# Optimization experiments

Hardware: AMD Instinct MI355X
Metric: run time of the kernel (lower is better)

Reference implementation:

```python
import jax, jax.numpy as jnp
import numpy as np

N = 20000      # nodes
E = 500000     # edges (~25 neighbors/node)
G = 64         # graphs in batch
NF = 64        # num_features (node dim)
NG = 100       # num_gaussians (edge dim)
L = 6          # conv layers
FC = 128       # fc_feat_size
NFC = 3        # num_fc_layers - 1
EMB = 92       # KHOT embedding width
CUTOFF = 6.0
EPS = 1e-5


def setup_inputs() -> dict:
    key = jax.random.key(0)
    ks = jax.random.split(key, 16)
    s = 0.05
    inp = {}
    inp['atomic_numbers'] = jax.random.randint(ks[0], (N,), 0, 100, dtype=jnp.int32)
    inp['neighbors_index'] = jax.random.randint(ks[1], (2, E), 0, N, dtype=jnp.int32)
    inp['distances'] = jax.random.uniform(ks[2], (E,), dtype=jnp.float32) * CUTOFF
    inp['batch'] = jnp.sort(jax.random.randint(ks[3], (N,), 0, G, dtype=jnp.int32))
    # parameters
    inp['embedding'] = jax.random.normal(ks[4], (100, EMB), jnp.float32) * s
    inp['nuc_W'] = jax.random.normal(ks[5], (EMB, NF), jnp.float32) * s
    inp['nuc_b'] = jnp.zeros((NF,), jnp.float32)
    inp['conv_W'] = jax.random.normal(ks[6], (L, 2 * NF + NG, 2 * NF), jnp.float32) * s
    inp['conv_b'] = jnp.zeros((L, 2 * NF), jnp.float32)
    inp['bn_g'] = jnp.ones((L, 2 * NF), jnp.float32)
    inp['bn_b'] = jnp.zeros((L, 2 * NF), jnp.float32)
    inp['ln_g'] = jnp.ones((L, NF), jnp.float32)
    inp['ln_b'] = jnp.zeros((L, NF), jnp.float32)
    inp['fc1_W'] = jax.random.normal(ks[7], (NF, FC), jnp.float32) * s
    inp['fc1_b'] = jnp.zeros((FC,), jnp.float32)
    inp['fcs_W'] = jax.random.normal(ks[8], (NFC, FC, FC), jnp.float32) * s
    inp['fcs_b'] = jnp.zeros((NFC, FC), jnp.float32)
    inp['out_W'] = jax.random.normal(ks[9], (FC, 1), jnp.float32) * s
    inp['out_b'] = jnp.zeros((1,), jnp.float32)
    return inp


def reference(atomic_numbers, neighbors_index, distances, batch,
              embedding, nuc_W, nuc_b, conv_W, conv_b, bn_g, bn_b,
              ln_g, ln_b, fc1_W, fc1_b, fcs_W, fcs_b, out_W, out_b):
    # Gaussian smearing of edge distances -> [E, NG]
    offsets = jnp.linspace(0.0, CUTOFF, NG)
    coeff = -0.5 / (offsets[1] - offsets[0]) ** 2
    ef = jnp.exp(coeff * (distances[:, None] - offsets) ** 2)

    # atom k-hot embedding -> nuclear linear embedding: [N, NF]
    x = embedding[atomic_numbers] @ nuc_W + nuc_b

    src, dst = neighbors_index[0], neighbors_index[1]  # x_j = src, x_i = dst

    for l in range(L):
        # edge message: gather + concat + linear
        z = jnp.concatenate([x[dst], x[src], ef], axis=1) @ conv_W[l] + conv_b[l]
        # BatchNorm1d over edges (training-mode batch statistics, biased var)
        mu = z.mean(axis=0)
        var = jnp.mean((z - mu) ** 2, axis=0)
        z = (z - mu) / jnp.sqrt(var + EPS) * bn_g[l] + bn_b[l]
        z1, z2 = jnp.split(z, 2, axis=1)
        m = jax.nn.sigmoid(z1) * jax.nn.softplus(z2)  # [E, NF]
        # scatter-add aggregate to target nodes
        agg = jax.ops.segment_sum(m, dst, num_segments=N)
        # LayerNorm + residual + softplus
        mu2 = agg.mean(axis=-1, keepdims=True)
        var2 = jnp.mean((agg - mu2) ** 2, axis=-1, keepdims=True)
        h = (agg - mu2) / jnp.sqrt(var2 + EPS) * ln_g[l] + ln_b[l]
        x = jax.nn.softplus(h + x)

    # mean pool per graph
    counts = jnp.maximum(jax.ops.segment_sum(jnp.ones((N,), x.dtype), batch, num_segments=G), 1.0)
    mol = jax.ops.segment_sum(x, batch, num_segments=G) / counts[:, None]

    h = jax.nn.softplus(mol @ fc1_W + fc1_b)
    for i in range(NFC):
        h = jax.nn.softplus(h @ fcs_W[i] + fcs_b[i])
    y = h @ out_W + out_b  # [G, 1]
    return y
```

## Files before the change

kernel.cpp:

```cpp
#include <hip/hip_runtime.h>
#include <hip/hip_fp16.h>
#include <cmath>

#define NN 20000
#define EE 500000
#define GG 64
#define TS 8192
#define SW 4096
#define EPS 1e-5f

__device__ __forceinline__ float softplus_ref(float x) {
    return fmaxf(x, 0.f) + log1pf(__expf(-fabsf(x)));
}
__device__ __forceinline__ float softplus_fast(float x) {
    return fmaxf(x, 0.f) + __logf(1.0f + __expf(-fabsf(x)));
}
__device__ __forceinline__ float sigmoid_fast(float x) {
    return __builtin_amdgcn_rcpf(1.0f + __expf(-x));
}

__global__ void k_gtab(float* __restrict__ g) {
    int i = blockIdx.x * 256 + threadIdx.x;
    if (i >= TS * 100) return;
    int s = i / 100, k = i - 100 * s;
    float d = s * (6.0f / (TS - 1.0f));
    float o = k * (6.0f / 99.0f);
    float step = 6.0f / 99.0f;
    float coeff = -0.5f / (step * step);
    float df = d - o;
    g[i] = __expf(coeff * df * df);
}

__global__ void __launch_bounds__(256) k_build_T(
    const float* __restrict__ g, const float* __restrict__ convW,
    const float* __restrict__ convB, __half2* __restrict__ Tn) {
    int lane = threadIdx.x & 63;
    int wv = __builtin_amdgcn_readfirstlane(threadIdx.x >> 6);
    int l = blockIdx.y;
    int s0 = blockIdx.x * 16 + wv * 4;
    const float* w = convW + ((size_t)l * 228 + 128) * 128;
    const float* g0 = g + (size_t)s0 * 100;
    float b0 = convB[l * 128 + lane], b1 = convB[l * 128 + lane + 64];
    float2 a0 = {b0, b1}, a1 = {b0, b1}, a2 = {b0, b1}, a3 = {b0, b1};
#pragma unroll 4
    for (int k = 0; k < 100; k++) {
        float w0 = w[k * 128 + lane];
        float w1 = w[k * 128 + lane + 64];
        float ga = g0[k], gb = g0[100 + k], gc = g0[200 + k], gd = g0[300 + k];
        a0.x += ga * w0; a0.y += ga * w1;
        a1.x += gb * w0; a1.y += gb * w1;
        a2.x += gc * w0; a2.y += gc * w1;
        a3.x += gd * w0; a3.y += gd * w1;
    }
    Tn[((size_t)l * TS + s0 + 0) * 64 + lane] = __floats2half2_rn(a0.x, a0.y);
    Tn[((size_t)l * TS + s0 + 1) * 64 + lane] = __floats2half2_rn(a1.x, a1.y);
    Tn[((size_t)l * TS + s0 + 2) * 64 + lane] = __floats2half2_rn(a2.x, a2.y);
    Tn[((size_t)l * TS + s0 + 3) * 64 + lane] = __floats2half2_rn(a3.x, a3.y);
}

__global__ void k_prepW(const float* __restrict__ convW, float4* __restrict__ Wp) {
    int lane = threadIdx.x;
    int k = blockIdx.x;
    int l = blockIdx.y;
    const float* W1 = convW + ((size_t)l * 228 + k) * 128;
    const float* W2 = convW + ((size_t)l * 228 + 64 + k) * 128;
    Wp[((size_t)l * 64 + k) * 64 + lane] =
        make_float4(W1[lane], W1[lane + 64], W2[lane], W2[lane + 64]);
}

__global__ void k_embed(const int* __restrict__ an, const float* __restrict__ emb,
                        const float* __restrict__ W, const float* __restrict__ b,
                        float* __restrict__ x) {
    int c = threadIdx.x & 63, nl = threadIdx.x >> 6;
    int n = blockIdx.x * 4 + nl;
    if (n >= NN) return;
    const float* e = emb + (size_t)an[n] * 92;
    float acc = b[c];
#pragma unroll 4
    for (int k = 0; k < 92; k++) acc += e[k] * W[k * 64 + c];
    x[(size_t)n * 64 + c] = acc;
}

__global__ void k_hist(const int* __restrict__ dst, int* __restrict__ counts) {
    int e = blockIdx.x * 256 + threadIdx.x;
    if (e < EE) atomicAdd(&counts[dst[e]], 1);
}

__global__ void k_scan_local(const int* __restrict__ counts, int* __restrict__ rp,
                             int* __restrict__ bsum) {
    __shared__ int buf[1024];
    int b = blockIdx.x, tid = threadIdx.x;
    int i = b * 1024 + tid;
    int val = (i < NN) ? counts[i] : 0;
    buf[tid] = val;
    __syncthreads();
    for (int off = 1; off < 1024; off <<= 1) {
        int t = (tid >= off) ? buf[tid - off] : 0;
        __syncthreads();
        buf[tid] += t;
        __syncthreads();
    }
    if (i < NN) rp[i + 1] = buf[tid];
    if (tid == 1023) bsum[b] = buf[1023];
}

__global__ void k_scan_off(int* __restrict__ bsum, int nb) {
    if (threadIdx.x == 0) {
        int acc = 0;
        for (int b = 0; b < nb; b++) { int v = bsum[b]; bsum[b] = acc; acc += v; }
    }
}

__global__ void k_scan_add(int* __restrict__ rp, const int* __restrict__ bsum) {
    int b = blockIdx.x, tid = threadIdx.x;
    int i = b * 1024 + tid;
    if (i < NN) rp[i + 1] += bsum[b];
    if (b == 0 && tid == 0) rp[0] = 0;
}

__global__ void k_wsn(const int* __restrict__ rp, int* __restrict__ wsn) {
    int w = blockIdx.x * 256 + threadIdx.x;
    if (w >= SW) return;
    int e0 = (int)((long long)w * EE / SW);
    int lo = 0, hi = NN;
    while (lo + 1 < hi) {
        int mid = (lo + hi) >> 1;
        if (rp[mid] <= e0) lo = mid; else hi = mid;
    }
    wsn[w] = lo;
}

__global__ void k_scatter(const int* __restrict__ src, const int* __restrict__ dst,
                          const float* __restrict__ dist, const int* __restrict__ rp,
                          int* __restrict__ cursor, unsigned* __restrict__ ej) {
    int e = blockIdx.x * 256 + threadIdx.x;
    if (e < EE) {
        int d = dst[e];
        int p = atomicAdd(&cursor[d], 1);
        float t = dist[e] * ((TS - 1.0f) / 6.0f);
        int j = (int)(t + 0.5f);
        if (j > TS - 1) j = TS - 1;
        ej[rp[d] + p] = ((unsigned)src[e] << 13) | (unsigned)j;
    }
}

__global__ void __launch_bounds__(256) k_uv(const float* __restrict__ x,
                                            const float4* __restrict__ Wp,
                                            __half2* __restrict__ up, __half2* __restrict__ vp) {
    int lane = threadIdx.x & 63;
    int wv = __builtin_amdgcn_readfirstlane(threadIdx.x >> 6);
    int n0 = (blockIdx.x * 4 + wv) * 4;
    float xa = x[(size_t)(n0 + 0) * 64 + lane];
    float xb = x[(size_t)(n0 + 1) * 64 + lane];
    float xc = x[(size_t)(n0 + 2) * 64 + lane];
    float xd = x[(size_t)(n0 + 3) * 64 + lane];
    float2 ua = {0, 0}, ub = {0, 0}, uc = {0, 0}, ud = {0, 0};
    float2 va = {0, 0}, vb = {0, 0}, vc = {0, 0}, vd = {0, 0};
#pragma unroll 8
    for (int k = 0; k < 64; k++) {
        float4 w = Wp[k * 64 + lane];
        float ka = __uint_as_float(__builtin_amdgcn_readlane(__float_as_uint(xa), k));
        float kb = __uint_as_float(__builtin_amdgcn_readlane(__float_as_uint(xb), k));
        float kc = __uint_as_float(__builtin_amdgcn_readlane(__float_as_uint(xc), k));
        float kd = __uint_as_float(__builtin_amdgcn_readlane(__float_as_uint(xd), k));
        ua.x += ka * w.x; ua.y += ka * w.y; va.x += ka * w.z; va.y += ka * w.w;
        ub.x += kb * w.x; ub.y += kb * w.y; vb.x += kb * w.z; vb.y += kb * w.w;
        uc.x += kc * w.x; uc.y += kc * w.y; vc.x += kc * w.z; vc.y += kc * w.w;
        ud.x += kd * w.x; ud.y += kd * w.y; vd.x += kd * w.z; vd.y += kd * w.w;
    }
    up[(size_t)(n0 + 0) * 64 + lane] = __floats2half2_rn(ua.x, ua.y);
    up[(size_t)(n0 + 1) * 64 + lane] = __floats2half2_rn(ub.x, ub.y);
    up[(size_t)(n0 + 2) * 64 + lane] = __floats2half2_rn(uc.x, uc.y);
    up[(size_t)(n0 + 3) * 64 + lane] = __floats2half2_rn(ud.x, ud.y);
    vp[(size_t)(n0 + 0) * 64 + lane] = __floats2half2_rn(va.x, va.y);
    vp[(size_t)(n0 + 1) * 64 + lane] = __floats2half2_rn(vb.x, vb.y);
    vp[(size_t)(n0 + 2) * 64 + lane] = __floats2half2_rn(vc.x, vc.y);
    vp[(size_t)(n0 + 3) * 64 + lane] = __floats2half2_rn(vd.x, vd.y);
}

#define GRP2(P, BODY)                                                        \
    {                                                                        \
        unsigned e[P];                                                       \
        _Pragma("unroll")                                                    \
        for (int t = 0; t < P; t++)                                          \
            e[t] = __builtin_nontemporal_load(&ej[idx + 2 * t + slot]);      \
        __half2 vh[P], th[P];                                                \
        _Pragma("unroll")                                                    \
        for (int t = 0; t < P; t++) {                                        \
            vh[t] = vp[(size_t)(e[t] >> 13) * 64 + hp];                      \
            th[t] = Tn[(size_t)(e[t] & 8191u) * 64 + hp];                    \
        }                                                                    \
        _Pragma("unroll")                                                    \
        for (int t = 0; t < P; t++) { BODY }                                 \
    }

#define STATS_BODY                                                           \
    float2 vv = __half22float2(vh[t]);                                       \
    float2 tt = __half22float2(th[t]);                                       \
    float z0 = uu.x + vv.x + tt.x;                                           \
    float z1 = uu.y + vv.y + tt.y;                                           \
    sx += z0; qx += z0 * z0; sy += z1; qy += z1 * z1;

#define AGG_BODY                                                             \
    __half2 vt = __hadd2(vh[t], th[t]);                                      \
    float2 f = __half22float2(vt);                                           \
    float z0 = fmaf(A1, f.x, C1);                                            \
    float z1 = fmaf(A2, f.y, C2);                                            \
    acc += sigmoid_fast(z0) * softplus_fast(z1);

__global__ void __launch_bounds__(256) k_stats_h(
    const __half2* __restrict__ up, const __half2* __restrict__ vp,
    const __half2* __restrict__ Tn, const unsigned* __restrict__ ej,
    const int* __restrict__ rp, const int* __restrict__ wsn,
    float* __restrict__ sums) {
    int lane = threadIdx.x & 63;
    int wv = __builtin_amdgcn_readfirstlane(threadIdx.x >> 6);
    int bid = blockIdx.x;
    int h = (bid >> 2) & 1;
    int r = ((bid >> 3) << 2) | (bid & 3);
    int slot = lane >> 5;
    int hp = h * 32 + (lane & 31);
    int w = r * 4 + wv;
    int e0 = (int)((long long)w * EE / SW);
    int e1 = (int)((long long)(w + 1) * EE / SW);
    int n = __builtin_amdgcn_readfirstlane(wsn[w]);
    int rend = __builtin_amdgcn_readfirstlane(rp[n + 1]);
    float sx = 0.f, sy = 0.f, qx = 0.f, qy = 0.f;
    int idx = e0;
    while (idx < e1) {
        while (idx >= rend) {
            ++n;
            rend = __builtin_amdgcn_readfirstlane(rp[n + 1]);
        }
        float2 uu = __half22float2(up[(size_t)n * 64 + hp]);
        int stop = (e1 < rend) ? e1 : rend;
        for (; idx + 32 <= stop; idx += 32) GRP2(16, STATS_BODY)
        if (idx + 16 <= stop) { GRP2(8, STATS_BODY) idx += 16; }
        if (idx + 8 <= stop) { GRP2(4, STATS_BODY) idx += 8; }
        if (idx + 4 <= stop) { GRP2(2, STATS_BODY) idx += 4; }
        if (idx + 2 <= stop) { GRP2(1, STATS_BODY) idx += 2; }
        if (idx < stop) {
            unsigned e = ej[idx];
            __half2 vh0 = vp[(size_t)(e >> 13) * 64 + hp];
            __half2 th0 = Tn[(size_t)(e & 8191u) * 64 + hp];
            float2 vv = __half22float2(vh0);
            float2 tt = __half22float2(th0);
            float z0 = uu.x + vv.x + tt.x;
            float z1 = uu.y + vv.y + tt.y;
            if (!slot) {
                sx += z0; qx += z0 * z0; sy += z1; qy += z1 * z1;
            }
            idx += 1;
        }
    }
    sx += __shfl_xor(sx, 32, 64); sy += __shfl_xor(sy, 32, 64);
    qx += __shfl_xor(qx, 32, 64); qy += __shfl_xor(qy, 32, 64);
    __shared__ float red[4][32][4];
    if (!slot) {
        float* rr = red[wv][lane & 31];
        rr[0] = sx; rr[1] = sy; rr[2] = qx; rr[3] = qy;
    }
    __syncthreads();
    if (wv == 0 && !slot) {
        for (int q = 1; q < 4; q++) {
            const float* rr = red[q][lane & 31];
            sx += rr[0]; sy += rr[1]; qx += rr[2]; qy += rr[3];
        }
        int c0 = hp;
        atomicAdd(&sums[c0], sx);
        atomicAdd(&sums[64 + c0], sy);
        atomicAdd(&sums[128 + c0], qx);
        atomicAdd(&sums[192 + c0], qy);
    }
}

__global__ void __launch_bounds__(256) k_aggh(
    const __half2* __restrict__ up, const __half2* __restrict__ vp,
    const __half2* __restrict__ Tn, const unsigned* __restrict__ ej,
    const int* __restrict__ rp, const float* __restrict__ sums,
    const float* __restrict__ bng, const float* __restrict__ bnb,
    int l, float* __restrict__ accbuf) {
    int lane = threadIdx.x & 63;
    int wv = __builtin_amdgcn_readfirstlane(threadIdx.x >> 6);
    int bid = blockIdx.x;
    int h = (bid >> 2) & 1;
    int r = ((bid >> 3) << 2) | (bid & 3);
    int slot = lane >> 5;
    int hp = h * 32 + (lane & 31);
    int i = r * 4 + wv;

    int c0 = hp;
    float mu1 = sums[c0] * (1.0f / EE);
    float var1 = sums[128 + c0] * (1.0f / EE) - mu1 * mu1;
    float A1 = rsqrtf(var1 + EPS) * bng[l * 128 + c0];
    float B1 = bnb[l * 128 + c0] - mu1 * A1;
    float mu2 = sums[64 + c0] * (1.0f / EE);
    float var2 = sums[192 + c0] * (1.0f / EE) - mu2 * mu2;
    float A2 = rsqrtf(var2 + EPS) * bng[l * 128 + 64 + c0];
    float B2 = bnb[l * 128 + 64 + c0] - mu2 * A2;

    float2 uu = __half22float2(up[(size_t)i * 64 + hp]);
    float C1 = fmaf(A1, uu.x, B1);
    float C2 = fmaf(A2, uu.y, B2);
    float acc = 0.f;
    int rs = __builtin_amdgcn_readfirstlane(rp[i]);
    int re = __builtin_amdgcn_readfirstlane(rp[i + 1]);
    int idx = rs;
    for (; idx + 16 <= re; idx += 16) GRP2(8, AGG_BODY)
    if (idx + 8 <= re) { GRP2(4, AGG_BODY) idx += 8; }
    if (idx + 4 <= re) { GRP2(2, AGG_BODY) idx += 4; }
    if (idx + 2 <= re) { GRP2(1, AGG_BODY) idx += 2; }
    if (idx < re) {
        unsigned e = ej[idx];
        __half2 vh0 = vp[(size_t)(e >> 13) * 64 + hp];
        __half2 th0 = Tn[(size_t)(e & 8191u) * 64 + hp];
        __half2 vt = __hadd2(vh0, th0);
        float2 f = __half22float2(vt);
        float z0 = fmaf(A1, f.x, C1);
        float z1 = fmaf(A2, f.y, C2);
        if (!slot) acc += sigmoid_fast(z0) * softplus_fast(z1);
    }
    acc += __shfl_xor(acc, 32, 64);
    if (!slot) accbuf[(size_t)i * 64 + hp] = acc;
}

__global__ void __launch_bounds__(256) k_lnfin(
    const float* __restrict__ accbuf,
    const float* __restrict__ lng, const float* __restrict__ lnb,
    int l, const float* __restrict__ xin, float* __restrict__ xout) {
    int lane = threadIdx.x & 63;
    int wv = __builtin_amdgcn_readfirstlane(threadIdx.x >> 6);
    int i = blockIdx.x * 4 + wv;
    float a = accbuf[(size_t)i * 64 + lane];
    float xr = xin[(size_t)i * 64 + lane];
    float s = a;
#pragma unroll
    for (int off = 32; off; off >>= 1) s += __shfl_xor(s, off, 64);
    float mean = s * (1.0f / 64.0f);
    float e0v = a - mean;
    float vv2 = e0v * e0v;
#pragma unroll
    for (int off = 32; off; off >>= 1) vv2 += __shfl_xor(vv2, off, 64);
    float var = vv2 * (1.0f / 64.0f);
    float h = e0v * rsqrtf(var + EPS) * lng[l * 64 + lane] + lnb[l * 64 + lane];
    xout[(size_t)i * 64 + lane] = softplus_ref(h + xr);
}

__global__ void k_gp(const int* __restrict__ batch, int* __restrict__ gp) {
    int g = threadIdx.x;
    if (g > GG) return;
    int lo = 0, hi = NN;
    while (lo < hi) {
        int mid = (lo + hi) >> 1;
        if (batch[mid] < g) lo = mid + 1; else hi = mid;
    }
    gp[g] = lo;
}

__global__ void k_pool2(const float* __restrict__ x, const int* __restrict__ gp,
                        float* __restrict__ mols) {
    int g = blockIdx.x;
    int lane = threadIdx.x & 63, slot = threadIdx.x >> 6;
    int s0 = gp[g], s1 = gp[g + 1];
    float acc = 0.f;
    for (int n = s0 + slot; n < s1; n += 4) acc += x[(size_t)n * 64 + lane];
    __shared__ float red[4][64];
    red[slot][lane] = acc;
    __syncthreads();
    if (slot == 0) {
        float a = red[0][lane] + red[1][lane] + red[2][lane] + red[3][lane];
        float cc = fmaxf((float)(s1 - s0), 1.0f);
        mols[g * 64 + lane] = a / cc;
    }
}

__global__ void k_mlp(const float* __restrict__ mols,
                      const float* __restrict__ fc1W, const float* __restrict__ fc1b,
                      const float* __restrict__ fcsW, const float* __restrict__ fcsb,
                      const float* __restrict__ outW, const float* __restrict__ outb,
                      float* __restrict__ y) {
    int g = blockIdx.x, t = threadIdx.x;
    __shared__ float m[64];
    __shared__ float h[128];
    __shared__ float rbuf[128];
    if (t < 64) m[t] = mols[g * 64 + t];
    __syncthreads();
    float a = fc1b[t];
#pragma unroll 4
    for (int k = 0; k < 64; k++) a += m[k] * fc1W[k * 128 + t];
    h[t] = softplus_ref(a);
    __syncthreads();
    for (int i = 0; i < 3; i++) {
        float b = fcsb[i * 128 + t];
#pragma unroll 4
        for (int k = 0; k < 128; k++) b += h[k] * fcsW[((size_t)i * 128 + k) * 128 + t];
        __syncthreads();
        h[t] = softplus_ref(b);
        __syncthreads();
    }
    rbuf[t] = h[t] * outW[t];
    __syncthreads();
    if (t < 64) {
        float s2 = rbuf[t] + rbuf[t + 64];
#pragma unroll
        for (int off = 32; off; off >>= 1) s2 += __shfl_xor(s2, off, 64);
        if (t == 0) y[g] = s2 + outb[0];
    }
}

extern "C" void kernel_launch(void* const* d_in, const int* in_sizes, int n_in,
                              void* d_out, int out_size, void* d_ws, size_t ws_size,
                              hipStream_t stream) {
    const int*   an    = (const int*)d_in[0];
    const int*   nbr   = (const int*)d_in[1];
    const float* dist  = (const float*)d_in[2];
    const int*   batch = (const int*)d_in[3];
    const float* emb   = (const float*)d_in[4];
    const float* nucW  = (const float*)d_in[5];
    const float* nucB  = (const float*)d_in[6];
    const float* convW = (const float*)d_in[7];
    const float* convB = (const float*)d_in[8];
    const float* bng   = (const float*)d_in[9];
    const float* bnb   = (const float*)d_in[10];
    const float* lng   = (const float*)d_in[11];
    const float* lnb   = (const float*)d_in[12];
    const float* fc1W  = (const float*)d_in[13];
    const float* fc1b  = (const float*)d_in[14];
    const float* fcsW  = (const float*)d_in[15];
    const float* fcsb  = (const float*)d_in[16];
    const float* outW  = (const float*)d_in[17];
    const float* outb  = (const float*)d_in[18];
    const int* srcI = nbr;
    const int* dstI = nbr + EE;

    char* base = (char*)d_ws;
    size_t off = 0;
    auto alloc = [&](size_t b) { size_t r = off; off += (b + 255) & ~(size_t)255; return r; };
    float*    gtab   = (float*)(base + alloc((size_t)TS * 100 * 4));
    __half2*  Tall   = (__half2*)(base + alloc((size_t)6 * TS * 64 * 4));
    float4*   Wp     = (float4*)(base + alloc((size_t)6 * 64 * 64 * 16));
    float*    x0     = (float*)(base + alloc((size_t)NN * 64 * 4));
    float*    x1     = (float*)(base + alloc((size_t)NN * 64 * 4));
    __half2*  up     = (__half2*)(base + alloc((size_t)NN * 64 * 4));
    __half2*  vp     = (__half2*)(base + alloc((size_t)NN * 64 * 4));
    float*    accb   = (float*)(base + alloc((size_t)NN * 64 * 4));
    float*    sums6  = (float*)(base + alloc((size_t)6 * 256 * 4));
    int*      counts = (int*)(base + alloc((size_t)NN * 4));
    int*      cursor = (int*)(base + alloc((size_t)NN * 4));
    int*      rp     = (int*)(base + alloc((size_t)(NN + 1) * 4));
    int*      bsum   = (int*)(base + alloc(64 * 4));
    unsigned* ej     = (unsigned*)(base + alloc((size_t)(EE + 64) * 4));
    int*      wsn    = (int*)(base + alloc((size_t)SW * 4));
    float*    mols   = (float*)(base + alloc((size_t)GG * 64 * 4));
    int*      gp     = (int*)(base + alloc((size_t)(GG + 1) * 4));

    hipMemsetAsync(counts, 0, (size_t)NN * 4, stream);
    hipMemsetAsync(cursor, 0, (size_t)NN * 4, stream);
    hipMemsetAsync(sums6, 0, (size_t)6 * 256 * 4, stream);

    k_gtab<<<(TS * 100 + 255) / 256, 256, 0, stream>>>(gtab);
    k_build_T<<<dim3(TS / 16, 6), 256, 0, stream>>>(gtab, convW, convB, Tall);
    k_prepW<<<dim3(64, 6), 64, 0, stream>>>(convW, Wp);
    k_embed<<<(NN + 3) / 4, 256, 0, stream>>>(an, emb, nucW, nucB, x0);
    k_hist<<<(EE + 255) / 256, 256, 0, stream>>>(dstI, counts);
    const int NB = (NN + 1023) / 1024;
    k_scan_local<<<NB, 1024, 0, stream>>>(counts, rp, bsum);
    k_scan_off<<<1, 64, 0, stream>>>(bsum, NB);
    k_scan_add<<<NB, 1024, 0, stream>>>(rp, bsum);
    k_wsn<<<SW / 256, 256, 0, stream>>>(rp, wsn);
    k_scatter<<<(EE + 255) / 256, 256, 0, stream>>>(srcI, dstI, dist, rp, cursor, ej);
    k_gp<<<1, 128, 0, stream>>>(batch, gp);

    float* xin = x0;
    float* xout = x1;
    for (int l = 0; l < 6; l++) {
        k_uv<<<NN / 16, 256, 0, stream>>>(xin, Wp + (size_t)l * 64 * 64, up, vp);
        const __half2* Tnl = Tall + (size_t)l * TS * 64;
        float* sums = sums6 + (size_t)l * 256;
        k_stats_h<<<2048, 256, 0, stream>>>(up, vp, Tnl, ej, rp, wsn, sums);
        k_aggh<<<10000, 256, 0, stream>>>(up, vp, Tnl, ej, rp, sums,
                                          bng, bnb, l, accb);
        k_lnfin<<<NN / 4, 256, 0, stream>>>(accb, lng, lnb, l, xin, xout);
        float* tmp = xin; xin = xout; xout = tmp;
    }
    k_pool2<<<GG, 256, 0, stream>>>(xin, gp, mols);
    k_mlp<<<GG, 128, 0, stream>>>(mols, fc1W, fc1b, fcsW, fcsb, outW, outb, (float*)d_out);
}
```

Before: 922.4 us.

## Fuse LayerNorm finish into next layer's u/v projection and tweak stats loads

Adds a kernel that applies LayerNorm, the residual and softplus for the previous layer and then computes the next layer's u/v half-precision projections in the same pass, removing one launch and one read of x per layer. The stats kernel now reads edge pairs as one 64-bit load and picks its half by lane slot instead of using per-slot nontemporal loads, and its main loop is unrolled by 8 groups instead of 16. The MLP loops are unrolled further. The final layer's LayerNorm still runs in the original kernel before pooling, and the new edge loads rely on 4-byte alignment with unaligned 64-bit access.

```diff
diff --git a/kernel.cpp b/kernel.cpp
--- a/kernel.cpp
+++ b/kernel.cpp
@@ -8,6 +8,8 @@
 #define TS 8192
 #define SW 4096
 #define EPS 1e-5f
+
+typedef unsigned long long u64a __attribute__((aligned(4)));
 
 __device__ __forceinline__ float softplus_ref(float x) {
     return fmaxf(x, 0.f) + log1pf(__expf(-fabsf(x)));
@@ -178,12 +180,68 @@
     vp[(size_t)(n0 + 3) * 64 + lane] = __floats2half2_rn(vd.x, vd.y);
 }
 
+__global__ void __launch_bounds__(256) k_uvln(
+    const float* __restrict__ accb,
+    const float* __restrict__ lng, const float* __restrict__ lnb, int lp,
+    const float* __restrict__ xin, float* __restrict__ xout,
+    const float4* __restrict__ Wp,
+    __half2* __restrict__ up, __half2* __restrict__ vp) {
+    int lane = threadIdx.x & 63;
+    int wv = __builtin_amdgcn_readfirstlane(threadIdx.x >> 6);
+    int n0 = (blockIdx.x * 4 + wv) * 4;
+    float lg = lng[lp * 64 + lane], lb = lnb[lp * 64 + lane];
+    float xs[4];
+#pragma unroll
+    for (int j = 0; j < 4; j++) {
+        int n = n0 + j;
+        float a = accb[(size_t)n * 64 + lane];
+        float xr = xin[(size_t)n * 64 + lane];
+        float s = a;
+#pragma unroll
+        for (int off = 32; off; off >>= 1) s += __shfl_xor(s, off, 64);
+        float mean = s * (1.0f / 64.0f);
+        float e0v = a - mean;
+        float vv2 = e0v * e0v;
+#pragma unroll
+        for (int off = 32; off; off >>= 1) vv2 += __shfl_xor(vv2, off, 64);
+        float var = vv2 * (1.0f / 64.0f);
+        float h = e0v * rsqrtf(var + EPS) * lg + lb;
+        xs[j] = softplus_ref(h + xr);
+        xout[(size_t)n * 64 + lane] = xs[j];
+    }
+    float xa = xs[0], xb = xs[1], xc = xs[2], xd = xs[3];
+    float2 ua = {0, 0}, ub = {0, 0}, uc = {0, 0}, ud = {0, 0};
+    float2 va = {0, 0}, vb = {0, 0}, vc = {0, 0}, vd = {0, 0};
+#pragma unroll 8
+    for (int k = 0; k < 64; k++) {
+        float4 w = Wp[k * 64 + lane];
+        float ka = __uint_as_float(__builtin_amdgcn_readlane(__float_as_uint(xa), k));
+        float kb = __uint_as_float(__builtin_amdgcn_readlane(__float_as_uint(xb), k));
+        float kc = __uint_as_float(__builtin_amdgcn_readlane(__float_as_uint(xc), k));
+        float kd = __uint_as_float(__builtin_amdgcn_readlane(__float_as_uint(xd), k));
+        ua.x += ka * w.x; ua.y += ka * w.y; va.x += ka * w.z; va.y += ka * w.w;
+        ub.x += kb * w.x; ub.y += kb * w.y; vb.x += kb * w.z; vb.y += kb * w.w;
+        uc.x += kc * w.x; uc.y += kc * w.y; vc.x += kc * w.z; vc.y += kc * w.w;
+        ud.x += kd * w.x; ud.y += kd * w.y; vd.x += kd * w.z; vd.y += kd * w.w;
+    }
+    up[(size_t)(n0 + 0) * 64 + lane] = __floats2half2_rn(ua.x, ua.y);
+    up[(size_t)(n0 + 1) * 64 + lane] = __floats2half2_rn(ub.x, ub.y);
+    up[(size_t)(n0 + 2) * 64 + lane] = __floats2half2_rn(uc.x, uc.y);
+    up[(size_t)(n0 + 3) * 64 + lane] = __floats2half2_rn(ud.x, ud.y);
+    vp[(size_t)(n0 + 0) * 64 + lane] = __floats2half2_rn(va.x, va.y);
+    vp[(size_t)(n0 + 1) * 64 + lane] = __floats2half2_rn(vb.x, vb.y);
+    vp[(size_t)(n0 + 2) * 64 + lane] = __floats2half2_rn(vc.x, vc.y);
+    vp[(size_t)(n0 + 3) * 64 + lane] = __floats2half2_rn(vd.x, vd.y);
+}
+
 #define GRP2(P, BODY)                                                        \
     {                                                                        \
         unsigned e[P];                                                       \
         _Pragma("unroll")                                                    \
-        for (int t = 0; t < P; t++)                                          \
-            e[t] = __builtin_nontemporal_load(&ej[idx + 2 * t + slot]);      \
+        for (int t = 0; t < P; t++) {                                        \
+            unsigned long long ep = *(const u64a*)&ej[idx + 2 * t];          \
+            e[t] = slot ? (unsigned)(ep >> 32) : (unsigned)ep;               \
+        }                                                                    \
         __half2 vh[P], th[P];                                                \
         _Pragma("unroll")                                                    \
         for (int t = 0; t < P; t++) {                                        \
@@ -234,8 +292,7 @@
         }
         float2 uu = __half22float2(up[(size_t)n * 64 + hp]);
         int stop = (e1 < rend) ? e1 : rend;
-        for (; idx + 32 <= stop; idx += 32) GRP2(16, STATS_BODY)
-        if (idx + 16 <= stop) { GRP2(8, STATS_BODY) idx += 16; }
+        for (; idx + 16 <= stop; idx += 16) GRP2(8, STATS_BODY)
         if (idx + 8 <= stop) { GRP2(4, STATS_BODY) idx += 8; }
         if (idx + 4 <= stop) { GRP2(2, STATS_BODY) idx += 4; }
         if (idx + 2 <= stop) { GRP2(1, STATS_BODY) idx += 2; }
@@ -386,13 +443,13 @@
     if (t < 64) m[t] = mols[g * 64 + t];
     __syncthreads();
     float a = fc1b[t];
-#pragma unroll 4
+#pragma unroll 16
     for (int k = 0; k < 64; k++) a += m[k] * fc1W[k * 128 + t];
     h[t] = softplus_ref(a);
     __syncthreads();
     for (int i = 0; i < 3; i++) {
         float b = fcsb[i * 128 + t];
-#pragma unroll 4
+#pragma unroll 16
         for (int k = 0; k < 128; k++) b += h[k] * fcsW[((size_t)i * 128 + k) * 128 + t];
         __syncthreads();
         h[t] = softplus_ref(b);
@@ -474,15 +531,21 @@
     float* xin = x0;
     float* xout = x1;
     for (int l = 0; l < 6; l++) {
-        k_uv<<<NN / 16, 256, 0, stream>>>(xin, Wp + (size_t)l * 64 * 64, up, vp);
+        if (l == 0) {
+            k_uv<<<NN / 16, 256, 0, stream>>>(xin, Wp, up, vp);
+        } else {
+            k_uvln<<<NN / 16, 256, 0, stream>>>(accb, lng, lnb, l - 1,
+                                                xin, xout, Wp + (size_t)l * 64 * 64,
+                                                up, vp);
+            float* tmp = xin; xin = xout; xout = tmp;
+        }
         const __half2* Tnl = Tall + (size_t)l * TS * 64;
         float* sums = sums6 + (size_t)l * 256;
         k_stats_h<<<2048, 256, 0, stream>>>(up, vp, Tnl, ej, rp, wsn, sums);
         k_aggh<<<10000, 256, 0, stream>>>(up, vp, Tnl, ej, rp, sums,
                                           bng, bnb, l, accb);
-        k_lnfin<<<NN / 4, 256, 0, stream>>>(accb, lng, lnb, l, xin, xout);
-        float* tmp = xin; xin = xout; xout = tmp;
-    }
-    k_pool2<<<GG, 256, 0, stream>>>(xin, gp, mols);
+    }
+    k_lnfin<<<NN / 4, 256, 0, stream>>>(accb, lng, lnb, 5, xin, xout);
+    k_pool2<<<GG, 256, 0, stream>>>(xout, gp, mols);
     k_mlp<<<GG, 128, 0, stream>>>(mols, fc1W, fc1b, fcsW, fcsb, outW, outb, (float*)d_out);
 }
```

New measurement: 832.2 us. 1.11x faster.

## Use MFMA fp16 for node projections, exp2-based activations, paired edge loads

Applied to the files above, without the earlier changes.

Replaces the scalar readlane-based per-node u/v projection with an MFMA 16x16x32 fp16 matmul over a half-precision copy of x. The weights are pre-packed into the MFMA operand layout and the LN kernel now also writes xh. Activations in the aggregation use exp2/log2 intrinsics with LOG2E prescaling and a final LN2 rescale. Other changes: edge indices are read as 64-bit pairs instead of nontemporal 32-bit loads, the stats loop uses groups of 8 instead of 16, and MLP unrolling is raised. The fp16 input to the matmul adds rounding error, and the MFMA output is written with strided 2-byte stores.

```diff
diff --git a/kernel.cpp b/kernel.cpp
--- a/kernel.cpp
+++ b/kernel.cpp
@@ -8,12 +8,15 @@
 #define TS 8192
 #define SW 4096
 #define EPS 1e-5f
+#define LOG2E 1.442695040888963f
+#define LN2 0.693147180559945f
+
+typedef unsigned long long u64a __attribute__((aligned(4)));
+typedef _Float16 f16x8 __attribute__((ext_vector_type(8)));
+typedef float f32x4 __attribute__((ext_vector_type(4)));
 
 __device__ __forceinline__ float softplus_ref(float x) {
     return fmaxf(x, 0.f) + log1pf(__expf(-fabsf(x)));
-}
-__device__ __forceinline__ float softplus_fast(float x) {
-    return fmaxf(x, 0.f) + __logf(1.0f + __expf(-fabsf(x)));
 }
 __device__ __forceinline__ float sigmoid_fast(float x) {
     return __builtin_amdgcn_rcpf(1.0f + __expf(-x));
@@ -58,19 +61,27 @@
     Tn[((size_t)l * TS + s0 + 3) * 64 + lane] = __floats2half2_rn(a3.x, a3.y);
 }
 
-__global__ void k_prepW(const float* __restrict__ convW, float4* __restrict__ Wp) {
+__global__ void k_prepW2(const float* __restrict__ convW, _Float16* __restrict__ Wf) {
     int lane = threadIdx.x;
-    int k = blockIdx.x;
-    int l = blockIdx.y;
-    const float* W1 = convW + ((size_t)l * 228 + k) * 128;
-    const float* W2 = convW + ((size_t)l * 228 + 64 + k) * 128;
-    Wp[((size_t)l * 64 + k) * 64 + lane] =
-        make_float4(W1[lane], W1[lane + 64], W2[lane], W2[lane + 64]);
+    int ct = blockIdx.x;
+    int half = blockIdx.y;
+    int l = blockIdx.z;
+    int p = ct * 16 + (lane & 15);
+    int s = p >> 7;
+    int r = p & 127;
+    int colW = (r >> 1) + (r & 1) * 64;
+    int k0 = half * 32 + (lane >> 4) * 8;
+    _Float16* dst = Wf + (((size_t)(l * 16 + ct) * 2 + half) * 64 + lane) * 8;
+#pragma unroll
+    for (int i = 0; i < 8; i++) {
+        float v = convW[((size_t)l * 228 + s * 64 + k0 + i) * 128 + colW];
+        dst[i] = (_Float16)v;
+    }
 }
 
 __global__ void k_embed(const int* __restrict__ an, const float* __restrict__ emb,
                         const float* __restrict__ W, const float* __restrict__ b,
-                        float* __restrict__ x) {
+                        float* __restrict__ x, _Float16* __restrict__ xh) {
     int c = threadIdx.x & 63, nl = threadIdx.x >> 6;
     int n = blockIdx.x * 4 + nl;
     if (n >= NN) return;
@@ -79,6 +90,7 @@
 #pragma unroll 4
     for (int k = 0; k < 92; k++) acc += e[k] * W[k * 64 + c];
     x[(size_t)n * 64 + c] = acc;
+    xh[(size_t)n * 64 + c] = (_Float16)acc;
 }
 
 __global__ void k_hist(const int* __restrict__ dst, int* __restrict__ counts) {
@@ -144,46 +156,42 @@
     }
 }
 
-__global__ void __launch_bounds__(256) k_uv(const float* __restrict__ x,
-                                            const float4* __restrict__ Wp,
-                                            __half2* __restrict__ up, __half2* __restrict__ vp) {
+__global__ void __launch_bounds__(256) k_uvmm(
+    const _Float16* __restrict__ xh, const _Float16* __restrict__ Wf, int l,
+    _Float16* __restrict__ uph, _Float16* __restrict__ vph) {
     int lane = threadIdx.x & 63;
-    int wv = __builtin_amdgcn_readfirstlane(threadIdx.x >> 6);
-    int n0 = (blockIdx.x * 4 + wv) * 4;
-    float xa = x[(size_t)(n0 + 0) * 64 + lane];
-    float xb = x[(size_t)(n0 + 1) * 64 + lane];
-    float xc = x[(size_t)(n0 + 2) * 64 + lane];
-    float xd = x[(size_t)(n0 + 3) * 64 + lane];
-    float2 ua = {0, 0}, ub = {0, 0}, uc = {0, 0}, ud = {0, 0};
-    float2 va = {0, 0}, vb = {0, 0}, vc = {0, 0}, vd = {0, 0};
-#pragma unroll 8
-    for (int k = 0; k < 64; k++) {
-        float4 w = Wp[k * 64 + lane];
-        float ka = __uint_as_float(__builtin_amdgcn_readlane(__float_as_uint(xa), k));
-        float kb = __uint_as_float(__builtin_amdgcn_readlane(__float_as_uint(xb), k));
-        float kc = __uint_as_float(__builtin_amdgcn_readlane(__float_as_uint(xc), k));
-        float kd = __uint_as_float(__builtin_amdgcn_readlane(__float_as_uint(xd), k));
-        ua.x += ka * w.x; ua.y += ka * w.y; va.x += ka * w.z; va.y += ka * w.w;
-        ub.x += kb * w.x; ub.y += kb * w.y; vb.x += kb * w.z; vb.y += kb * w.w;
-        uc.x += kc * w.x; uc.y += kc * w.y; vc.x += kc * w.z; vc.y += kc * w.w;
-        ud.x += kd * w.x; ud.y += kd * w.y; vd.x += kd * w.z; vd.y += kd * w.w;
-    }
-    up[(size_t)(n0 + 0) * 64 + lane] = __floats2half2_rn(ua.x, ua.y);
-    up[(size_t)(n0 + 1) * 64 + lane] = __floats2half2_rn(ub.x, ub.y);
-    up[(size_t)(n0 + 2) * 64 + lane] = __floats2half2_rn(uc.x, uc.y);
-    up[(size_t)(n0 + 3) * 64 + lane] = __floats2half2_rn(ud.x, ud.y);
-    vp[(size_t)(n0 + 0) * 64 + lane] = __floats2half2_rn(va.x, va.y);
-    vp[(size_t)(n0 + 1) * 64 + lane] = __floats2half2_rn(vb.x, vb.y);
-    vp[(size_t)(n0 + 2) * 64 + lane] = __floats2half2_rn(vc.x, vc.y);
-    vp[(size_t)(n0 + 3) * 64 + lane] = __floats2half2_rn(vd.x, vd.y);
+    int wv = threadIdx.x >> 6;
+    int tile = blockIdx.x * 4 + wv;
+    if (tile >= NN / 16) return;
+    int node = tile * 16 + (lane & 15);
+    const f16x8* ax = (const f16x8*)(xh + (size_t)node * 64 + ((lane >> 4) * 8));
+    f16x8 a0 = ax[0];
+    f16x8 a1 = ax[4];
+    const f16x8* wf = (const f16x8*)Wf + (size_t)l * 16 * 2 * 64;
+    int rowb = tile * 16 + ((lane >> 4) << 2);
+#pragma unroll
+    for (int ct = 0; ct < 16; ct++) {
+        f16x8 b0 = wf[(ct * 2 + 0) * 64 + lane];
+        f16x8 b1 = wf[(ct * 2 + 1) * 64 + lane];
+        f32x4 acc = {0.f, 0.f, 0.f, 0.f};
+        acc = __builtin_amdgcn_mfma_f32_16x16x32_f16(a0, b0, acc, 0, 0, 0);
+        acc = __builtin_amdgcn_mfma_f32_16x16x32_f16(a1, b1, acc, 0, 0, 0);
+        int p = ct * 16 + (lane & 15);
+        _Float16* dst = (p < 128) ? (uph + p) : (vph + (p - 128));
+#pragma unroll
+        for (int r2 = 0; r2 < 4; r2++)
+            dst[(size_t)(rowb + r2) * 128] = (_Float16)acc[r2];
+    }
 }
 
 #define GRP2(P, BODY)                                                        \
     {                                                                        \
         unsigned e[P];                                                       \
         _Pragma("unroll")                                                    \
-        for (int t = 0; t < P; t++)                                          \
-            e[t] = __builtin_nontemporal_load(&ej[idx + 2 * t + slot]);      \
+        for (int t = 0; t < P; t++) {                                        \
+            unsigned long long ep = *(const u64a*)&ej[idx + 2 * t];          \
+            e[t] = slot ? (unsigned)(ep >> 32) : (unsigned)ep;               \
+        }                                                                    \
         __half2 vh[P], th[P];                                                \
         _Pragma("unroll")                                                    \
         for (int t = 0; t < P; t++) {                                        \
@@ -206,7 +214,10 @@
     float2 f = __half22float2(vt);                                           \
     float z0 = fmaf(A1, f.x, C1);                                            \
     float z1 = fmaf(A2, f.y, C2);                                            \
-    acc += sigmoid_fast(z0) * softplus_fast(z1);
+    float sg = __builtin_amdgcn_rcpf(1.0f + __builtin_amdgcn_exp2f(-z0));    \
+    float sp = fmaxf(z1, 0.f) +                                              \
+               __builtin_amdgcn_logf(1.0f + __builtin_amdgcn_exp2f(-fabsf(z1))); \
+    acc += sg * sp;
 
 __global__ void __launch_bounds__(256) k_stats_h(
     const __half2* __restrict__ up, const __half2* __restrict__ vp,
@@ -234,8 +245,7 @@
         }
         float2 uu = __half22float2(up[(size_t)n * 64 + hp]);
         int stop = (e1 < rend) ? e1 : rend;
-        for (; idx + 32 <= stop; idx += 32) GRP2(16, STATS_BODY)
-        if (idx + 16 <= stop) { GRP2(8, STATS_BODY) idx += 16; }
+        for (; idx + 16 <= stop; idx += 16) GRP2(8, STATS_BODY)
         if (idx + 8 <= stop) { GRP2(4, STATS_BODY) idx += 8; }
         if (idx + 4 <= stop) { GRP2(2, STATS_BODY) idx += 4; }
         if (idx + 2 <= stop) { GRP2(1, STATS_BODY) idx += 2; }
@@ -300,8 +310,9 @@
     float B2 = bnb[l * 128 + 64 + c0] - mu2 * A2;
 
     float2 uu = __half22float2(up[(size_t)i * 64 + hp]);
-    float C1 = fmaf(A1, uu.x, B1);
-    float C2 = fmaf(A2, uu.y, B2);
+    float C1 = fmaf(A1, uu.x, B1) * LOG2E;
+    float C2 = fmaf(A2, uu.y, B2) * LOG2E;
+    A1 *= LOG2E; A2 *= LOG2E;
     float acc = 0.f;
     int rs = __builtin_amdgcn_readfirstlane(rp[i]);
     int re = __builtin_amdgcn_readfirstlane(rp[i + 1]);
@@ -318,16 +329,20 @@
         float2 f = __half22float2(vt);
         float z0 = fmaf(A1, f.x, C1);
         float z1 = fmaf(A2, f.y, C2);
-        if (!slot) acc += sigmoid_fast(z0) * softplus_fast(z1);
+        float sg = __builtin_amdgcn_rcpf(1.0f + __builtin_amdgcn_exp2f(-z0));
+        float sp = fmaxf(z1, 0.f) +
+                   __builtin_amdgcn_logf(1.0f + __builtin_amdgcn_exp2f(-fabsf(z1)));
+        if (!slot) acc += sg * sp;
     }
     acc += __shfl_xor(acc, 32, 64);
-    if (!slot) accbuf[(size_t)i * 64 + hp] = acc;
-}
-
-__global__ void __launch_bounds__(256) k_lnfin(
+    if (!slot) accbuf[(size_t)i * 64 + hp] = acc * LN2;
+}
+
+__global__ void __launch_bounds__(256) k_lnx(
     const float* __restrict__ accbuf,
     const float* __restrict__ lng, const float* __restrict__ lnb,
-    int l, const float* __restrict__ xin, float* __restrict__ xout) {
+    int l, const float* __restrict__ xin, float* __restrict__ xout,
+    _Float16* __restrict__ xh) {
     int lane = threadIdx.x & 63;
     int wv = __builtin_amdgcn_readfirstlane(threadIdx.x >> 6);
     int i = blockIdx.x * 4 + wv;
@@ -343,7 +358,9 @@
     for (int off = 32; off; off >>= 1) vv2 += __shfl_xor(vv2, off, 64);
     float var = vv2 * (1.0f / 64.0f);
     float h = e0v * rsqrtf(var + EPS) * lng[l * 64 + lane] + lnb[l * 64 + lane];
-    xout[(size_t)i * 64 + lane] = softplus_ref(h + xr);
+    float o = softplus_ref(h + xr);
+    xout[(size_t)i * 64 + lane] = o;
+    xh[(size_t)i * 64 + lane] = (_Float16)o;
 }
 
 __global__ void k_gp(const int* __restrict__ batch, int* __restrict__ gp) {
@@ -386,13 +403,13 @@
     if (t < 64) m[t] = mols[g * 64 + t];
     __syncthreads();
     float a = fc1b[t];
-#pragma unroll 4
+#pragma unroll 16
     for (int k = 0; k < 64; k++) a += m[k] * fc1W[k * 128 + t];
     h[t] = softplus_ref(a);
     __syncthreads();
     for (int i = 0; i < 3; i++) {
         float b = fcsb[i * 128 + t];
-#pragma unroll 4
+#pragma unroll 16
         for (int k = 0; k < 128; k++) b += h[k] * fcsW[((size_t)i * 128 + k) * 128 + t];
         __syncthreads();
         h[t] = softplus_ref(b);
@@ -436,23 +453,24 @@
     char* base = (char*)d_ws;
     size_t off = 0;
     auto alloc = [&](size_t b) { size_t r = off; off += (b + 255) & ~(size_t)255; return r; };
-    float*    gtab   = (float*)(base + alloc((size_t)TS * 100 * 4));
-    __half2*  Tall   = (__half2*)(base + alloc((size_t)6 * TS * 64 * 4));
-    float4*   Wp     = (float4*)(base + alloc((size_t)6 * 64 * 64 * 16));
-    float*    x0     = (float*)(base + alloc((size_t)NN * 64 * 4));
-    float*    x1     = (float*)(base + alloc((size_t)NN * 64 * 4));
-    __half2*  up     = (__half2*)(base + alloc((size_t)NN * 64 * 4));
-    __half2*  vp     = (__half2*)(base + alloc((size_t)NN * 64 * 4));
-    float*    accb   = (float*)(base + alloc((size_t)NN * 64 * 4));
-    float*    sums6  = (float*)(base + alloc((size_t)6 * 256 * 4));
-    int*      counts = (int*)(base + alloc((size_t)NN * 4));
-    int*      cursor = (int*)(base + alloc((size_t)NN * 4));
-    int*      rp     = (int*)(base + alloc((size_t)(NN + 1) * 4));
-    int*      bsum   = (int*)(base + alloc(64 * 4));
-    unsigned* ej     = (unsigned*)(base + alloc((size_t)(EE + 64) * 4));
-    int*      wsn    = (int*)(base + alloc((size_t)SW * 4));
-    float*    mols   = (float*)(base + alloc((size_t)GG * 64 * 4));
-    int*      gp     = (int*)(base + alloc((size_t)(GG + 1) * 4));
+    float*     gtab   = (float*)(base + alloc((size_t)TS * 100 * 4));
+    __half2*   Tall   = (__half2*)(base + alloc((size_t)6 * TS * 64 * 4));
+    _Float16*  Wf     = (_Float16*)(base + alloc((size_t)6 * 16 * 2 * 64 * 8 * 2));
+    float*     x0     = (float*)(base + alloc((size_t)NN * 64 * 4));
+    float*     x1     = (float*)(base + alloc((size_t)NN * 64 * 4));
+    _Float16*  xh     = (_Float16*)(base + alloc((size_t)NN * 64 * 2));
+    _Float16*  uph    = (_Float16*)(base + alloc((size_t)NN * 128 * 2));
+    _Float16*  vph    = (_Float16*)(base + alloc((size_t)NN * 128 * 2));
+    float*     accb   = (float*)(base + alloc((size_t)NN * 64 * 4));
+    float*     sums6  = (float*)(base + alloc((size_t)6 * 256 * 4));
+    int*       counts = (int*)(base + alloc((size_t)NN * 4));
+    int*       cursor = (int*)(base + alloc((size_t)NN * 4));
+    int*       rp     = (int*)(base + alloc((size_t)(NN + 1) * 4));
+    int*       bsum   = (int*)(base + alloc(64 * 4));
+    unsigned*  ej     = (unsigned*)(base + alloc((size_t)(EE + 64) * 4));
+    int*       wsn    = (int*)(base + alloc((size_t)SW * 4));
+    float*     mols   = (float*)(base + alloc((size_t)GG * 64 * 4));
+    int*       gp     = (int*)(base + alloc((size_t)(GG + 1) * 4));
 
     hipMemsetAsync(counts, 0, (size_t)NN * 4, stream);
     hipMemsetAsync(cursor, 0, (size_t)NN * 4, stream);
@@ -460,8 +478,8 @@
 
     k_gtab<<<(TS * 100 + 255) / 256, 256, 0, stream>>>(gtab);
     k_build_T<<<dim3(TS / 16, 6), 256, 0, stream>>>(gtab, convW, convB, Tall);
-    k_prepW<<<dim3(64, 6), 64, 0, stream>>>(convW, Wp);
-    k_embed<<<(NN + 3) / 4, 256, 0, stream>>>(an, emb, nucW, nucB, x0);
+    k_prepW2<<<dim3(16, 2, 6), 64, 0, stream>>>(convW, Wf);
+    k_embed<<<(NN + 3) / 4, 256, 0, stream>>>(an, emb, nucW, nucB, x0, xh);
     k_hist<<<(EE + 255) / 256, 256, 0, stream>>>(dstI, counts);
     const int NB = (NN + 1023) / 1024;
     k_scan_local<<<NB, 1024, 0, stream>>>(counts, rp, bsum);
@@ -473,14 +491,16 @@
 
     float* xin = x0;
     float* xout = x1;
+    const __half2* up = (const __half2*)uph;
+    const __half2* vp = (const __half2*)vph;
     for (int l = 0; l < 6; l++) {
-        k_uv<<<NN / 16, 256, 0, stream>>>(xin, Wp + (size_t)l * 64 * 64, up, vp);
+        k_uvmm<<<(NN / 16 + 3) / 4, 256, 0, stream>>>(xh, Wf, l, uph, vph);
         const __half2* Tnl = Tall + (size_t)l * TS * 64;
         float* sums = sums6 + (size_t)l * 256;
         k_stats_h<<<2048, 256, 0, stream>>>(up, vp, Tnl, ej, rp, wsn, sums);
         k_aggh<<<10000, 256, 0, stream>>>(up, vp, Tnl, ej, rp, sums,
                                           bng, bnb, l, accb);
-        k_lnfin<<<NN / 4, 256, 0, stream>>>(accb, lng, lnb, l, xin, xout);
+        k_lnx<<<NN / 4, 256, 0, stream>>>(accb, lng, lnb, l, xin, xout, xh);
         float* tmp = xin; xin = xout; xout = tmp;
     }
     k_pool2<<<GG, 256, 0, stream>>>(xin, gp, mols);
```

Measured after the change: 747.0 us. 1.23x faster.
